# Kernel optimization log

Measured on AMD Instinct MI355X. Metric: run time of the kernel, lower is better.

## Reference

```python
import jax, jax.numpy as jnp
import numpy as np
import math

B, S, D, H, HD = 2, 2048, 2048, 16, 128
ROPE_THETA = 10000.0


def _rope_cache(seq_len, dim, base, dtype=jnp.float32):
    inv_freq = 1.0 / (base ** (jnp.arange(0, dim, 2, dtype=jnp.float32) / dim))
    t = jnp.arange(seq_len, dtype=jnp.float32)
    freqs = jnp.einsum('i,j->ij', t, inv_freq)          # [S, dim/2]
    emb = jnp.concatenate([freqs, freqs], axis=-1)       # [S, dim]
    return jnp.cos(emb).astype(dtype), jnp.sin(emb).astype(dtype)


def _rotate_half(x):
    x1, x2 = x[..., : x.shape[-1] // 2], x[..., x.shape[-1] // 2:]
    return jnp.concatenate([-x2, x1], axis=-1)


def setup_inputs() -> dict:
    key = jax.random.key(0)
    ks = jax.random.split(key, 6)
    hidden_states = jax.random.normal(ks[0], (B, S, D), dtype=jnp.float32) * 0.02
    w_scale = 1.0 / math.sqrt(D)
    Wq = jax.random.normal(ks[1], (D, D), dtype=jnp.float32) * w_scale
    Wk = jax.random.normal(ks[2], (D, D), dtype=jnp.float32) * w_scale
    Wv = jax.random.normal(ks[3], (D, D), dtype=jnp.float32) * w_scale
    Wo = jax.random.normal(ks[4], (D, D), dtype=jnp.float32) * w_scale
    # additive causal mask [B, 1, S, S]: 0 on/below diag, large negative above
    causal = jnp.tril(jnp.ones((S, S), dtype=bool))
    attention_mask = jnp.where(causal, 0.0, -1e9).astype(jnp.float32)
    attention_mask = jnp.broadcast_to(attention_mask[None, None], (B, 1, S, S))
    position_ids = jnp.broadcast_to(jnp.arange(S, dtype=jnp.int32)[None], (B, S))
    return {
        'hidden_states': hidden_states,
        'attention_mask': attention_mask,
        'position_ids': position_ids,
        'Wq': Wq, 'Wk': Wk, 'Wv': Wv, 'Wo': Wo,
    }


def reference(hidden_states, attention_mask, position_ids, Wq, Wk, Wv, Wo):
    bsz, q_len, _ = hidden_states.shape
    # projections (torch Linear: x @ W.T), then split heads -> [B, H, S, HD]
    def proj(W):
        return jnp.einsum('bsd,ed->bse', hidden_states, W).reshape(bsz, q_len, H, HD).transpose(0, 2, 1, 3)
    q, k, v = proj(Wq), proj(Wk), proj(Wv)
    cos_c, sin_c = _rope_cache(q_len, HD, ROPE_THETA, hidden_states.dtype)
    cos = cos_c[position_ids][:, None]  # [B, 1, S, HD]
    sin = sin_c[position_ids][:, None]
    q = q * cos + _rotate_half(q) * sin
    k = k * cos + _rotate_half(k) * sin
    scores = jnp.einsum('bhqd,bhkd->bhqk', q, k) / math.sqrt(HD)
    scores = scores + attention_mask
    attn_weights = jax.nn.softmax(scores.astype(jnp.float32), axis=-1).astype(q.dtype)
    attn_out = jnp.einsum('bhqk,bhkd->bhqd', attn_weights, v)
    attn_out = attn_out.transpose(0, 2, 1, 3).reshape(bsz, q_len, D)
    out = jnp.einsum('bsd,ed->bse', attn_out, Wo)
    return out
```

## Files before the change

kernel.cpp:

```cpp
#include <hip/hip_runtime.h>

typedef __bf16 bf16;
typedef __bf16 bf16x8 __attribute__((ext_vector_type(8)));
typedef float f32x4 __attribute__((ext_vector_type(4)));

#define D_MODEL 2048
#define SEQ 2048
#define NH 16
#define HEAD_DIM 128
#define NBATCH 2
#define SM_SCALE 0.08838834764831845f
#define WSEG 4194304
#define NT_TILES 32

typedef __attribute__((address_space(1))) const void* gas_cp;
typedef __attribute__((address_space(3))) void* las_p;
__device__ __forceinline__ void ll16(const bf16* g, bf16* l) {
  __builtin_amdgcn_global_load_lds((gas_cp)g, (las_p)l, 16, 0, 0);
}

__device__ __forceinline__ bf16x8 cvt8(const float* p) {
  float4 a = *(const float4*)p;
  float4 b = *(const float4*)(p + 4);
  bf16x8 v;
  v[0] = (bf16)a.x; v[1] = (bf16)a.y; v[2] = (bf16)a.z; v[3] = (bf16)a.w;
  v[4] = (bf16)b.x; v[5] = (bf16)b.y; v[6] = (bf16)b.z; v[7] = (bf16)b.w;
  return v;
}

__global__ __launch_bounds__(256)
void cvt_hidden(const float* __restrict__ src, bf16* __restrict__ dst) {
  size_t i = ((size_t)blockIdx.x * 256 + threadIdx.x) * 8;
  *(bf16x8*)(dst + i) = cvt8(src + i);
}

__global__ __launch_bounds__(256)
void cvt_weights(const float* __restrict__ w0, const float* __restrict__ w1,
                 const float* __restrict__ w2, const float* __restrict__ w3,
                 bf16* __restrict__ dst) {
  const float* src = (blockIdx.y == 0) ? w0 : (blockIdx.y == 1) ? w1
                   : (blockIdx.y == 2) ? w2 : w3;
  size_t i = ((size_t)blockIdx.x * 256 + threadIdx.x) * 8;
  *(bf16x8*)(dst + (size_t)blockIdx.y * WSEG + i) = cvt8(src + i);
}

#define LDF256(DA, DB, SB, KX)                                               \
  _Pragma("unroll") for (int mi = 0; mi < 8; mi++)                           \
      DA[mi] = *(const bf16x8*)((SB) + ((arowQ + mi * 16) << 7) + (KX));     \
  DB[0] = *(const bf16x8*)((SB) + 32768 + (qb0 << 7) + (KX));                \
  DB[1] = *(const bf16x8*)((SB) + 32768 + (qb1 << 7) + (KX));                \
  DB[2] = *(const bf16x8*)((SB) + 32768 + (qb2 << 7) + (KX));                \
  DB[3] = *(const bf16x8*)((SB) + 32768 + (qb3 << 7) + (KX));

#define MM256(AF, BF)                                                        \
  _Pragma("unroll") for (int mi = 0; mi < 8; mi++)                           \
  _Pragma("unroll") for (int ni = 0; ni < 4; ni++)                           \
      acc[mi][ni] = __builtin_amdgcn_mfma_f32_16x16x32_bf16(                 \
          AF[mi], BF[ni], acc[mi][ni], 0, 0, 0);

#define ST2(GP, ROW0, KT, LB)                                                \
  ll16((GP) + (size_t)((ROW0) + w * 8 + l8) * D_MODEL + (KT) * 64 + kelem,   \
       (bf16*)((LB) + w * 1024));

__global__ __launch_bounds__(512, 2)
void gemm256(const bf16* __restrict__ A, const bf16* __restrict__ W,
             bf16* __restrict__ Qo, bf16* __restrict__ Ko,
             bf16* __restrict__ Vo, const int* __restrict__ pos_ids) {
  __shared__ __align__(16) char smem[131072];

  const int tid  = threadIdx.x;
  const int lane = tid & 63;
  const int w    = tid >> 6;
  const int quad = lane >> 4, l15 = lane & 15;
  const int l8   = lane >> 3, l7 = lane & 7;
  const int kelem = 8 * (l7 ^ l8);
  const int wm2 = w >> 2;
  const int wn2 = w & 3;
  const int hh  = wn2 >> 1;
  const int cb  = (wn2 & 1) * 32;

  const int bid = blockIdx.x;
  const int lin = (bid & 7) * 48 + (bid >> 3);
  const int by = lin / 24, bx = lin % 24;
  const int mBase = by << 8, nBase = bx << 8;

  const int kx0 = (quad * 16) ^ ((l15 & 7) << 4);
  const int kx1 = kx0 ^ 64;
  const int arowQ = wm2 * 128 + l15;
  const int qb0 = hh * 128 + cb + l15;
  const int qb1 = qb0 + 16, qb2 = qb0 + 64, qb3 = qb0 + 80;

  f32x4 acc[8][4];
#pragma unroll
  for (int i = 0; i < 8; i++)
#pragma unroll
    for (int j = 0; j < 4; j++) acc[i][j] = 0.0f;

  bf16x8 aP[8], bP[4];
  bf16x8 aQ[8], bQ[4];

  {
    char* s0 = smem;
    ST2(A, mBase,       0, s0 + 0);
    ST2(A, mBase + 64,  0, s0 + 8192);
    ST2(A, mBase + 128, 0, s0 + 16384);
    ST2(A, mBase + 192, 0, s0 + 24576);
    ST2(W, nBase,       0, s0 + 32768);
    ST2(W, nBase + 64,  0, s0 + 40960);
    ST2(W, nBase + 128, 0, s0 + 49152);
    ST2(W, nBase + 192, 0, s0 + 57344);
  }
  asm volatile("s_waitcnt vmcnt(0)" ::: "memory");
  __builtin_amdgcn_s_barrier();
  LDF256(aP, bP, smem, kx0);

  int buf = 0;
  for (int t = 0; t < NT_TILES; ++t) {
    char* const Sb = smem + buf * 65536;
    char* const Ob = smem + (buf ^ 1) * 65536;
    const bool pf  = (t + 1 < NT_TILES);

    LDF256(aQ, bQ, Sb, kx1);
    if (pf) {
      ST2(A, mBase,       t + 1, Ob + 0);
      ST2(A, mBase + 64,  t + 1, Ob + 8192);
      ST2(A, mBase + 128, t + 1, Ob + 16384);
      ST2(A, mBase + 192, t + 1, Ob + 24576);
      ST2(W, nBase,       t + 1, Ob + 32768);
      ST2(W, nBase + 64,  t + 1, Ob + 40960);
      ST2(W, nBase + 128, t + 1, Ob + 49152);
      ST2(W, nBase + 192, t + 1, Ob + 57344);
    }
    __builtin_amdgcn_sched_barrier(0);
    __builtin_amdgcn_s_setprio(1);
    MM256(aP, bP);
    __builtin_amdgcn_s_setprio(0);
    asm volatile("s_waitcnt lgkmcnt(0)" ::: "memory");
    asm volatile("s_waitcnt vmcnt(0)" ::: "memory");
    __builtin_amdgcn_s_barrier();

    if (pf) {
      LDF256(aP, bP, Ob, kx0);
    }
    __builtin_amdgcn_sched_barrier(0);
    __builtin_amdgcn_s_setprio(1);
    MM256(aQ, bQ);
    __builtin_amdgcn_s_setprio(0);
    asm volatile("s_waitcnt lgkmcnt(0)" ::: "memory");

    buf ^= 1;
  }

  const int matrix = nBase >> 11;
  const int nb     = nBase & 2047;
  if (matrix == 2) {
    const int h = (nb >> 7) + hh;
#pragma unroll
    for (int mi = 0; mi < 8; mi++)
#pragma unroll
      for (int ni = 0; ni < 4; ni++) {
        const int hd = cb + (ni & 1) * 16 + (ni >> 1) * 64 + l15;
#pragma unroll
        for (int r = 0; r < 4; r++) {
          int m = mBase + wm2 * 128 + mi * 16 + quad * 4 + r;
          int b = m >> 11, s2 = m & 2047;
          Vo[((size_t)((b * NH + h) * HEAD_DIM + hd)) * SEQ + s2] =
              (bf16)acc[mi][ni][r];
        }
      }
  } else {
    bf16* Out = (matrix == 0) ? Qo : Ko;
    float invf[2];
#pragma unroll
    for (int ni = 0; ni < 2; ni++)
      invf[ni] = __expf(-(float)(cb + ni * 16 + l15) *
                        (9.210340371976184f / 64.0f));
#pragma unroll
    for (int mi = 0; mi < 8; mi++)
#pragma unroll
      for (int r = 0; r < 4; r++) {
        int m = mBase + wm2 * 128 + mi * 16 + quad * 4 + r;
        float pos = (float)pos_ids[m];
        bf16* op = Out + (size_t)m * D_MODEL + nb + hh * 128 + cb + l15;
#pragma unroll
        for (int ni = 0; ni < 2; ni++) {
          float sn, cs;
          __sincosf(pos * invf[ni], &sn, &cs);
          float q0 = acc[mi][ni][r];
          float q1 = acc[mi][ni + 2][r];
          op[ni * 16]      = (bf16)(q0 * cs - q1 * sn);
          op[ni * 16 + 64] = (bf16)(q1 * cs + q0 * sn);
        }
      }
  }
}

#define LDFRAG(DA, DB, SB, KX)                                               \
  _Pragma("unroll") for (int mi = 0; mi < 4; mi++)                           \
      DA[mi] = *(const bf16x8*)((SB) + ((arow + mi * 16) << 7) + (KX));      \
  DB[0] = *(const bf16x8*)((SB) + 16384 + (rb0 << 7) + (KX));                \
  DB[1] = *(const bf16x8*)((SB) + 16384 + (rb1 << 7) + (KX));                \
  DB[2] = *(const bf16x8*)((SB) + 16384 + (rb2 << 7) + (KX));                \
  DB[3] = *(const bf16x8*)((SB) + 16384 + (rb3 << 7) + (KX));

#define MMAC(AF, BF)                                                         \
  _Pragma("unroll") for (int mi = 0; mi < 4; mi++)                           \
  _Pragma("unroll") for (int ni = 0; ni < 4; ni++)                           \
      acc[mi][ni] = __builtin_amdgcn_mfma_f32_16x16x32_bf16(                 \
          AF[mi], BF[ni], acc[mi][ni], 0, 0, 0);

#define ST1(GP, ROW0, KT, LB)                                                \
  ll16((GP) + (size_t)((ROW0) + w * 8 + l8) * D_MODEL + (KT) * 64 + kelem,   \
       (bf16*)((LB) + w * 1024));

__global__ __launch_bounds__(512, 2)
void gemm_proj(const bf16* __restrict__ A, const bf16* __restrict__ W,
               float* __restrict__ C) {
  __shared__ __align__(16) char smem[147456];

  const int tid  = threadIdx.x;
  const int lane = tid & 63;
  const int w    = tid >> 6;
  const int quad = lane >> 4, l15 = lane & 15;
  const int l8   = lane >> 3, l7 = lane & 7;
  const int kelem = 8 * (l7 ^ l8);
  const int wm = w >> 2;
  const int wn = w & 3;

  const int bid = blockIdx.x;
  const int lin = (bid & 7) * 32 + (bid >> 3);
  const int by = lin >> 3, bx = lin & 7;
  const int mBase = by << 7, nBase = bx << 8;

  const int kx0 = (quad * 16) ^ ((l15 & 7) << 4);
  const int kx1 = kx0 ^ 64;
  const int arow = wm * 64 + l15;
  const int rb0 = wn * 64 + l15;
  const int rb1 = rb0 + 16, rb2 = rb0 + 32, rb3 = rb0 + 48;

  f32x4 acc[4][4];
#pragma unroll
  for (int i = 0; i < 4; i++)
#pragma unroll
    for (int j = 0; j < 4; j++) acc[i][j] = 0.0f;

  bf16x8 aP[4], bP[4], aQ[4], bQ[4];

  {
    char* s0 = smem;
    char* s1 = smem + 49152;
    ST1(A, mBase,       0, s0 + 0);
    ST1(A, mBase + 64,  0, s0 + 8192);
    ST1(W, nBase,       0, s0 + 16384);
    ST1(W, nBase + 64,  0, s0 + 24576);
    ST1(W, nBase + 128, 0, s0 + 32768);
    ST1(W, nBase + 192, 0, s0 + 40960);
    ST1(A, mBase,       1, s1 + 0);
    ST1(A, mBase + 64,  1, s1 + 8192);
    ST1(W, nBase,       1, s1 + 16384);
    ST1(W, nBase + 64,  1, s1 + 24576);
    ST1(W, nBase + 128, 1, s1 + 32768);
    ST1(W, nBase + 192, 1, s1 + 40960);
  }
  asm volatile("s_waitcnt vmcnt(6)" ::: "memory");
  __builtin_amdgcn_s_barrier();
  LDFRAG(aP, bP, smem, kx0);

  int buf = 0;
  for (int t = 0; t < NT_TILES; ++t) {
    char* const Sb  = smem + buf * 49152;
    const int  nb1  = (buf + 1 == 3) ? 0 : buf + 1;
    const int  pb   = (buf + 2 >= 3) ? buf - 1 : buf + 2;
    char* const Nb  = smem + nb1 * 49152;
    char* const Pb  = smem + pb * 49152;
    const bool pf   = (t + 2 < NT_TILES);

    LDFRAG(aQ, bQ, Sb, kx1);
    if (pf) {
      ST1(A, mBase,      t + 2, Pb + 0);
      ST1(A, mBase + 64, t + 2, Pb + 8192);
      ST1(W, nBase,      t + 2, Pb + 16384);
    }
    __builtin_amdgcn_sched_barrier(0);
    __builtin_amdgcn_s_setprio(1);
    MMAC(aP, bP);
    __builtin_amdgcn_s_setprio(0);
    asm volatile("s_waitcnt lgkmcnt(0)" ::: "memory");
    if (pf)
      asm volatile("s_waitcnt vmcnt(3)" ::: "memory");
    else
      asm volatile("s_waitcnt vmcnt(0)" ::: "memory");
    __builtin_amdgcn_s_barrier();

    if (t + 1 < NT_TILES) {
      LDFRAG(aP, bP, Nb, kx0);
    }
    if (pf) {
      ST1(W, nBase + 64,  t + 2, Pb + 24576);
      ST1(W, nBase + 128, t + 2, Pb + 32768);
      ST1(W, nBase + 192, t + 2, Pb + 40960);
    }
    __builtin_amdgcn_sched_barrier(0);
    __builtin_amdgcn_s_setprio(1);
    MMAC(aQ, bQ);
    __builtin_amdgcn_s_setprio(0);
    asm volatile("s_waitcnt lgkmcnt(0)" ::: "memory");
    __builtin_amdgcn_s_barrier();

    buf = nb1;
  }

#pragma unroll
  for (int mi = 0; mi < 4; mi++) {
    const int m = mBase + wm * 64 + mi * 16 + quad * 4;
#pragma unroll
    for (int ni = 0; ni < 4; ni++) {
      const int n = nBase + wn * 64 + ni * 16 + l15;
      float* cp = C + (size_t)m * D_MODEL + n;
#pragma unroll
      for (int r = 0; r < 4; r++) cp[(size_t)r * D_MODEL] = acc[mi][ni][r];
    }
  }
}

__global__ __launch_bounds__(512, 2)
void attn_v2(const bf16* __restrict__ Q, const bf16* __restrict__ K,
             const bf16* __restrict__ Vt, bf16* __restrict__ O) {
  __shared__ __align__(16) bf16 Kl[2][64 * 128];
  __shared__ __align__(16) bf16 Vl[2][128 * 64];
  __shared__ __align__(16) bf16 P_lds[128 * 72];

  const int tid  = threadIdx.x;
  const int lane = tid & 63;
  const int w    = tid >> 6;
  const int quad = lane >> 4, l15 = lane & 15;
  const int l8   = lane >> 3, l7 = lane & 7;
  const int qi   = 15 - (int)blockIdx.y;
  const int bh   = blockIdx.x;
  const size_t qkBase = (size_t)(bh >> 4) * SEQ * D_MODEL + (size_t)(bh & 15) * HEAD_DIM;
  const size_t vBase  = (size_t)bh * HEAD_DIM * SEQ;

  const int qbw  = qi * 128 + w * 16;
  const int prow = w * 16;
  const int kswz = (l15 & 7) << 3;

  bf16x8 qa[4];
#pragma unroll
  for (int kk = 0; kk < 4; kk++)
    qa[kk] = *(const bf16x8*)(Q + qkBase + (size_t)(qbw + l15) * D_MODEL + kk * 32 + quad * 8);

  bf16x8 ones;
#pragma unroll
  for (int i = 0; i < 8; i++) ones[i] = (bf16)1.0f;

  f32x4 oacc[8], ls;
#pragma unroll
  for (int ni = 0; ni < 8; ni++) oacc[ni] = 0.0f;
  ls = 0.0f;

  const int nt = 2 * qi + 2;

#define STAGE_KV(T0, BUF)                                                    \
  _Pragma("unroll") for (int i_ = 0; i_ < 2; i_++) {                         \
    const int u_ = w * 2 + i_;                                               \
    const int rK = u_ * 4 + quad;                                            \
    ll16(K + qkBase + (size_t)((T0) + rK) * D_MODEL + 8 * (l15 ^ (rK & 7)),  \
         &Kl[BUF][u_ * 512]);                                                \
    const int rV = u_ * 8 + l8;                                              \
    ll16(Vt + vBase + (size_t)rV * SEQ + (T0) + 8 * (l7 ^ (rV & 7)),         \
         &Vl[BUF][u_ * 512]);                                                \
  }

  STAGE_KV(0, 0);
  asm volatile("s_waitcnt vmcnt(0)" ::: "memory");
  __builtin_amdgcn_s_barrier();

  int cur = 0;
  for (int tt = 0; tt < nt; ++tt, cur ^= 1) {
    const int t0 = tt * 64;
    if (tt + 1 < nt) STAGE_KV(t0 + 64, cur ^ 1);

    if (t0 <= qbw + 15) {
      const bf16* Kc = &Kl[cur][0];
      const bf16* Vc = &Vl[cur][0];

      f32x4 sacc[4];
#pragma unroll
      for (int ni = 0; ni < 4; ni++) sacc[ni] = 0.0f;
#pragma unroll
      for (int kk = 0; kk < 4; kk++) {
#pragma unroll
        for (int ni = 0; ni < 4; ni++) {
          bf16x8 kf = *(const bf16x8*)&Kc[(ni * 16 + l15) * 128 +
                                          (((kk * 32 + quad * 8)) ^ kswz)];
          sacc[ni] = __builtin_amdgcn_mfma_f32_16x16x32_bf16(qa[kk], kf, sacc[ni], 0, 0, 0);
        }
      }

      if (t0 + 63 > qbw) {
#pragma unroll
        for (int r = 0; r < 4; r++) {
          int qrow = qbw + quad * 4 + r;
#pragma unroll
          for (int ni = 0; ni < 4; ni++) {
            int tcol = t0 + ni * 16 + l15;
            float pv = (tcol <= qrow) ? __expf(fminf(sacc[ni][r] * SM_SCALE, 30.0f)) : 0.0f;
            P_lds[(prow + quad * 4 + r) * 72 + ni * 16 + l15] = (bf16)pv;
          }
        }
      } else {
#pragma unroll
        for (int r = 0; r < 4; r++)
#pragma unroll
          for (int ni = 0; ni < 4; ni++)
            P_lds[(prow + quad * 4 + r) * 72 + ni * 16 + l15] =
                (bf16)__expf(fminf(sacc[ni][r] * SM_SCALE, 30.0f));
      }

#pragma unroll
      for (int kk2 = 0; kk2 < 2; kk2++) {
        bf16x8 pf = *(const bf16x8*)&P_lds[(prow + l15) * 72 + kk2 * 32 + quad * 8];
#pragma unroll
        for (int ni = 0; ni < 8; ni++) {
          bf16x8 vf = *(const bf16x8*)&Vc[(ni * 16 + l15) * 64 +
                                          (((kk2 * 32 + quad * 8)) ^ kswz)];
          oacc[ni] = __builtin_amdgcn_mfma_f32_16x16x32_bf16(pf, vf, oacc[ni], 0, 0, 0);
        }
        ls = __builtin_amdgcn_mfma_f32_16x16x32_bf16(pf, ones, ls, 0, 0, 0);
      }
    }

    asm volatile("s_waitcnt vmcnt(0)" ::: "memory");
    __builtin_amdgcn_s_barrier();
  }
#undef STAGE_KV

#pragma unroll
  for (int r = 0; r < 4; r++) {
    float inv = 1.0f / ls[r];
    bf16* op = O + qkBase + (size_t)(qbw + quad * 4 + r) * D_MODEL;
#pragma unroll
    for (int ni = 0; ni < 8; ni++)
      op[ni * 16 + l15] = (bf16)(oacc[ni][r] * inv);
  }
}

extern "C" void kernel_launch(void* const* d_in, const int* in_sizes, int n_in,
                              void* d_out, int out_size, void* d_ws, size_t ws_size,
                              hipStream_t stream) {
  const float* hidden = (const float*)d_in[0];
  const int* pos = (const int*)d_in[2];
  const float* Wq = (const float*)d_in[3];
  const float* Wk = (const float*)d_in[4];
  const float* Wv = (const float*)d_in[5];
  const float* Wo = (const float*)d_in[6];
  float* out = (float*)d_out;

  const size_t TENS = (size_t)NBATCH * SEQ * D_MODEL;
  bf16* Qb = (bf16*)d_ws;
  bf16* Kb = Qb + TENS;
  bf16* Vt = Kb + TENS;
  bf16* AO = Vt + TENS;
  bf16* Hb = AO + TENS;
  bf16* Wb = Hb + TENS;

  cvt_hidden<<<dim3(TENS / 2048), dim3(256), 0, stream>>>(hidden, Hb);
  cvt_weights<<<dim3(WSEG / 2048, 4), dim3(256), 0, stream>>>(Wq, Wk, Wv, Wo, Wb);

  gemm256<<<dim3(384), dim3(512), 0, stream>>>(Hb, Wb, Qb, Kb, Vt, pos);

  attn_v2<<<dim3(NBATCH * NH, 16), dim3(512), 0, stream>>>(Qb, Kb, Vt, AO);

  gemm_proj<<<dim3(256), dim3(512), 0, stream>>>(
      AO, Wb + 3 * (size_t)WSEG, out);
}
```

Baseline: 364.3 us.

## Restructure attention to 4-wave blocks processing paired causal q-tiles

The attention kernel now uses 256 threads (4 waves) per block, with each wave handling 32 query rows using two MFMA row tiles. The goal is to reuse every K/V LDS fragment across two query sub-tiles. Each block processes a complementary pair of q-tiles (15-j and j) in sequence to balance causal work, and the grid is halved to 8 in y. The P buffer is now swizzled with XOR instead of padded. In exchange the kernel carries more registers per wave, gets lower occupancy from launch_bounds(256,1), and runs fewer waves to hide latency.

Measured after the change: 377.9 us. 1.04x slower.

```diff
diff --git a/kernel.cpp b/kernel.cpp
--- a/kernel.cpp
+++ b/kernel.cpp
@@ -323,46 +323,32 @@
   }
 }
 
-__global__ __launch_bounds__(512, 2)
-void attn_v2(const bf16* __restrict__ Q, const bf16* __restrict__ K,
+__global__ __launch_bounds__(256, 1)
+void attn_v3(const bf16* __restrict__ Q, const bf16* __restrict__ K,
              const bf16* __restrict__ Vt, bf16* __restrict__ O) {
   __shared__ __align__(16) bf16 Kl[2][64 * 128];
   __shared__ __align__(16) bf16 Vl[2][128 * 64];
-  __shared__ __align__(16) bf16 P_lds[128 * 72];
+  __shared__ __align__(16) bf16 Pl[128 * 64];
 
   const int tid  = threadIdx.x;
   const int lane = tid & 63;
   const int w    = tid >> 6;
   const int quad = lane >> 4, l15 = lane & 15;
   const int l8   = lane >> 3, l7 = lane & 7;
-  const int qi   = 15 - (int)blockIdx.y;
+  const int jj   = blockIdx.y;
   const int bh   = blockIdx.x;
   const size_t qkBase = (size_t)(bh >> 4) * SEQ * D_MODEL + (size_t)(bh & 15) * HEAD_DIM;
   const size_t vBase  = (size_t)bh * HEAD_DIM * SEQ;
-
-  const int qbw  = qi * 128 + w * 16;
-  const int prow = w * 16;
   const int kswz = (l15 & 7) << 3;
-
-  bf16x8 qa[4];
-#pragma unroll
-  for (int kk = 0; kk < 4; kk++)
-    qa[kk] = *(const bf16x8*)(Q + qkBase + (size_t)(qbw + l15) * D_MODEL + kk * 32 + quad * 8);
+  const int prow = w * 32;
 
   bf16x8 ones;
 #pragma unroll
   for (int i = 0; i < 8; i++) ones[i] = (bf16)1.0f;
 
-  f32x4 oacc[8], ls;
-#pragma unroll
-  for (int ni = 0; ni < 8; ni++) oacc[ni] = 0.0f;
-  ls = 0.0f;
-
-  const int nt = 2 * qi + 2;
-
 #define STAGE_KV(T0, BUF)                                                    \
-  _Pragma("unroll") for (int i_ = 0; i_ < 2; i_++) {                         \
-    const int u_ = w * 2 + i_;                                               \
+  _Pragma("unroll") for (int i_ = 0; i_ < 4; i_++) {                         \
+    const int u_ = w * 4 + i_;                                               \
     const int rK = u_ * 4 + quad;                                            \
     ll16(K + qkBase + (size_t)((T0) + rK) * D_MODEL + 8 * (l15 ^ (rK & 7)),  \
          &Kl[BUF][u_ * 512]);                                                \
@@ -371,78 +357,119 @@
          &Vl[BUF][u_ * 512]);                                                \
   }
 
-  STAGE_KV(0, 0);
-  asm volatile("s_waitcnt vmcnt(0)" ::: "memory");
-  __builtin_amdgcn_s_barrier();
-
-  int cur = 0;
-  for (int tt = 0; tt < nt; ++tt, cur ^= 1) {
-    const int t0 = tt * 64;
-    if (tt + 1 < nt) STAGE_KV(t0 + 64, cur ^ 1);
-
-    if (t0 <= qbw + 15) {
-      const bf16* Kc = &Kl[cur][0];
-      const bf16* Vc = &Vl[cur][0];
-
-      f32x4 sacc[4];
-#pragma unroll
-      for (int ni = 0; ni < 4; ni++) sacc[ni] = 0.0f;
-#pragma unroll
-      for (int kk = 0; kk < 4; kk++) {
-#pragma unroll
-        for (int ni = 0; ni < 4; ni++) {
-          bf16x8 kf = *(const bf16x8*)&Kc[(ni * 16 + l15) * 128 +
-                                          (((kk * 32 + quad * 8)) ^ kswz)];
-          sacc[ni] = __builtin_amdgcn_mfma_f32_16x16x32_bf16(qa[kk], kf, sacc[ni], 0, 0, 0);
+#pragma unroll 1
+  for (int ss = 0; ss < 2; ++ss) {
+    const int s   = ss ? jj : 15 - jj;
+    const int qbw = s * 128 + prow;
+    const int nt  = 2 * s + 2;
+
+    bf16x8 qa[2][4];
+#pragma unroll
+    for (int mi = 0; mi < 2; mi++)
+#pragma unroll
+      for (int kk = 0; kk < 4; kk++)
+        qa[mi][kk] = *(const bf16x8*)(Q + qkBase +
+            (size_t)(qbw + mi * 16 + l15) * D_MODEL + kk * 32 + quad * 8);
+
+    f32x4 oacc[2][8], ls[2];
+#pragma unroll
+    for (int mi = 0; mi < 2; mi++) {
+#pragma unroll
+      for (int ni = 0; ni < 8; ni++) oacc[mi][ni] = 0.0f;
+      ls[mi] = 0.0f;
+    }
+
+    STAGE_KV(0, 0);
+    asm volatile("s_waitcnt vmcnt(0)" ::: "memory");
+    __builtin_amdgcn_s_barrier();
+
+    int cur = 0;
+    for (int tt = 0; tt < nt; ++tt, cur ^= 1) {
+      const int t0 = tt * 64;
+      if (tt + 1 < nt) STAGE_KV(t0 + 64, cur ^ 1);
+
+      if (t0 <= qbw + 31) {
+        const bf16* Kc = &Kl[cur][0];
+        const bf16* Vc = &Vl[cur][0];
+
+        f32x4 sacc[2][4];
+#pragma unroll
+        for (int mi = 0; mi < 2; mi++)
+#pragma unroll
+          for (int ni = 0; ni < 4; ni++) sacc[mi][ni] = 0.0f;
+#pragma unroll
+        for (int kk = 0; kk < 4; kk++) {
+#pragma unroll
+          for (int ni = 0; ni < 4; ni++) {
+            bf16x8 kf = *(const bf16x8*)&Kc[(ni * 16 + l15) * 128 +
+                                            ((kk * 32 + quad * 8) ^ kswz)];
+            sacc[0][ni] = __builtin_amdgcn_mfma_f32_16x16x32_bf16(qa[0][kk], kf, sacc[0][ni], 0, 0, 0);
+            sacc[1][ni] = __builtin_amdgcn_mfma_f32_16x16x32_bf16(qa[1][kk], kf, sacc[1][ni], 0, 0, 0);
+          }
+        }
+
+        if (t0 + 63 > qbw) {
+#pragma unroll
+          for (int mi = 0; mi < 2; mi++)
+#pragma unroll
+            for (int r = 0; r < 4; r++) {
+              const int qrow = qbw + mi * 16 + quad * 4 + r;
+              const int prr  = prow + mi * 16 + quad * 4 + r;
+              const int rsw  = ((quad * 4 + r) & 7) << 3;
+#pragma unroll
+              for (int ni = 0; ni < 4; ni++) {
+                int tcol = t0 + ni * 16 + l15;
+                float pv = (tcol <= qrow)
+                    ? __expf(fminf(sacc[mi][ni][r] * SM_SCALE, 30.0f)) : 0.0f;
+                Pl[prr * 64 + ((ni * 16 + l15) ^ rsw)] = (bf16)pv;
+              }
+            }
+        } else {
+#pragma unroll
+          for (int mi = 0; mi < 2; mi++)
+#pragma unroll
+            for (int r = 0; r < 4; r++) {
+              const int prr = prow + mi * 16 + quad * 4 + r;
+              const int rsw = ((quad * 4 + r) & 7) << 3;
+#pragma unroll
+              for (int ni = 0; ni < 4; ni++)
+                Pl[prr * 64 + ((ni * 16 + l15) ^ rsw)] =
+                    (bf16)__expf(fminf(sacc[mi][ni][r] * SM_SCALE, 30.0f));
+            }
+        }
+
+#pragma unroll
+        for (int kk2 = 0; kk2 < 2; kk2++) {
+          const int pcol = (kk2 * 32 + quad * 8) ^ kswz;
+          bf16x8 pf0 = *(const bf16x8*)&Pl[(prow + l15) * 64 + pcol];
+          bf16x8 pf1 = *(const bf16x8*)&Pl[(prow + 16 + l15) * 64 + pcol];
+#pragma unroll
+          for (int ni = 0; ni < 8; ni++) {
+            bf16x8 vf = *(const bf16x8*)&Vc[(ni * 16 + l15) * 64 + pcol];
+            oacc[0][ni] = __builtin_amdgcn_mfma_f32_16x16x32_bf16(pf0, vf, oacc[0][ni], 0, 0, 0);
+            oacc[1][ni] = __builtin_amdgcn_mfma_f32_16x16x32_bf16(pf1, vf, oacc[1][ni], 0, 0, 0);
+          }
+          ls[0] = __builtin_amdgcn_mfma_f32_16x16x32_bf16(pf0, ones, ls[0], 0, 0, 0);
+          ls[1] = __builtin_amdgcn_mfma_f32_16x16x32_bf16(pf1, ones, ls[1], 0, 0, 0);
         }
       }
 
-      if (t0 + 63 > qbw) {
-#pragma unroll
-        for (int r = 0; r < 4; r++) {
-          int qrow = qbw + quad * 4 + r;
-#pragma unroll
-          for (int ni = 0; ni < 4; ni++) {
-            int tcol = t0 + ni * 16 + l15;
-            float pv = (tcol <= qrow) ? __expf(fminf(sacc[ni][r] * SM_SCALE, 30.0f)) : 0.0f;
-            P_lds[(prow + quad * 4 + r) * 72 + ni * 16 + l15] = (bf16)pv;
-          }
-        }
-      } else {
-#pragma unroll
-        for (int r = 0; r < 4; r++)
-#pragma unroll
-          for (int ni = 0; ni < 4; ni++)
-            P_lds[(prow + quad * 4 + r) * 72 + ni * 16 + l15] =
-                (bf16)__expf(fminf(sacc[ni][r] * SM_SCALE, 30.0f));
+      asm volatile("s_waitcnt vmcnt(0)" ::: "memory");
+      __builtin_amdgcn_s_barrier();
+    }
+
+#pragma unroll
+    for (int mi = 0; mi < 2; mi++)
+#pragma unroll
+      for (int r = 0; r < 4; r++) {
+        float inv = 1.0f / ls[mi][r];
+        bf16* op = O + qkBase + (size_t)(qbw + mi * 16 + quad * 4 + r) * D_MODEL;
+#pragma unroll
+        for (int ni = 0; ni < 8; ni++)
+          op[ni * 16 + l15] = (bf16)(oacc[mi][ni][r] * inv);
       }
-
-#pragma unroll
-      for (int kk2 = 0; kk2 < 2; kk2++) {
-        bf16x8 pf = *(const bf16x8*)&P_lds[(prow + l15) * 72 + kk2 * 32 + quad * 8];
-#pragma unroll
-        for (int ni = 0; ni < 8; ni++) {
-          bf16x8 vf = *(const bf16x8*)&Vc[(ni * 16 + l15) * 64 +
-                                          (((kk2 * 32 + quad * 8)) ^ kswz)];
-          oacc[ni] = __builtin_amdgcn_mfma_f32_16x16x32_bf16(pf, vf, oacc[ni], 0, 0, 0);
-        }
-        ls = __builtin_amdgcn_mfma_f32_16x16x32_bf16(pf, ones, ls, 0, 0, 0);
-      }
-    }
-
-    asm volatile("s_waitcnt vmcnt(0)" ::: "memory");
-    __builtin_amdgcn_s_barrier();
   }
 #undef STAGE_KV
-
-#pragma unroll
-  for (int r = 0; r < 4; r++) {
-    float inv = 1.0f / ls[r];
-    bf16* op = O + qkBase + (size_t)(qbw + quad * 4 + r) * D_MODEL;
-#pragma unroll
-    for (int ni = 0; ni < 8; ni++)
-      op[ni * 16 + l15] = (bf16)(oacc[ni][r] * inv);
-  }
 }
 
 extern "C" void kernel_launch(void* const* d_in, const int* in_sizes, int n_in,
@@ -469,7 +496,7 @@
 
   gemm256<<<dim3(384), dim3(512), 0, stream>>>(Hb, Wb, Qb, Kb, Vt, pos);
 
-  attn_v2<<<dim3(NBATCH * NH, 16), dim3(512), 0, stream>>>(Qb, Kb, Vt, AO);
+  attn_v3<<<dim3(NBATCH * NH, 8), dim3(256), 0, stream>>>(Qb, Kb, Vt, AO);
 
   gemm_proj<<<dim3(256), dim3(512), 0, stream>>>(
       AO, Wb + 3 * (size_t)WSEG, out);
```
